# Optimization experiments

Measured on AMD Instinct MI355X. Metric: run time of the kernel, lower is better.

Reference implementation:

```python
import jax, jax.numpy as jnp
import numpy as np

N = 50000        # nodes
E = 800000       # edges (avg degree 16)
D_IN = 128
HID = 128
K = 3


def cheb_edge_weights(row, col, n):
    # PyG ChebConv sym normalization with assumed lambda_max = 2.0:
    # L_hat = (2/lambda_max) * (I - D^-1/2 A D^-1/2) - I = -D^-1/2 A D^-1/2 (zero diagonal)
    mask = (row != col).astype(jnp.float32)  # remove_self_loops
    deg = jax.ops.segment_sum(mask, row, num_segments=n)
    dinv = jnp.where(deg > 0.0, jax.lax.rsqrt(jnp.maximum(deg, 1.0)), 0.0)
    return -dinv[row] * dinv[col] * mask  # [E]


def cheb_conv(x, row, col, w_edge, W, b, n):
    # Chebyshev recursion: Tx0=x, Tx1=L_hat x, Tx_k = 2 L_hat Tx_{k-1} - Tx_{k-2}
    def prop(h):  # sparse L_hat @ h via gather + segment_sum
        return jax.ops.segment_sum(w_edge[:, None] * h[col], row, num_segments=n)

    Tx0 = x
    out = Tx0 @ W[0]
    Tx1 = prop(Tx0)
    out = out + Tx1 @ W[1]
    for k in range(2, W.shape[0]):
        Tx2 = 2.0 * prop(Tx1) - Tx0
        out = out + Tx2 @ W[k]
        Tx0, Tx1 = Tx1, Tx2
    return out + b


def setup_inputs() -> dict:
    key = jax.random.key(0)
    ks = jax.random.split(key, 8)
    x = jax.random.normal(ks[0], (N, D_IN), dtype=jnp.float32)
    ei = jax.random.randint(ks[1], (2, E), 0, N, dtype=jnp.int32)
    s = 0.05
    W1 = jax.random.normal(ks[2], (K, D_IN, HID), dtype=jnp.float32) * s
    b1 = jnp.zeros((HID,), dtype=jnp.float32)
    W2 = jax.random.normal(ks[3], (K, HID, HID), dtype=jnp.float32) * s
    b2 = jnp.zeros((HID,), dtype=jnp.float32)
    W3 = jax.random.normal(ks[4], (K, HID, HID), dtype=jnp.float32) * s
    b3 = jnp.zeros((HID,), dtype=jnp.float32)
    return {"x": x, "ei": ei, "W1": W1, "b1": b1, "W2": W2, "b2": b2, "W3": W3, "b3": b3}


def reference(x, ei, W1, b1, W2, b2, W3, b3):
    row, col = ei[0], ei[1]
    w_edge = cheb_edge_weights(row, col, N)
    # layer chain: ChebConv -> ReLU -> dropout (eval mode: identity)
    h = jax.nn.relu(cheb_conv(x, row, col, w_edge, W1, b1, N))
    h = jax.nn.relu(cheb_conv(h, row, col, w_edge, W2, b2, N))
    h = jax.nn.relu(cheb_conv(h, row, col, w_edge, W3, b3, N))
    return h
```

## Files before the change

kernel.cpp:

```cpp
#include <hip/hip_runtime.h>
#include <hip/hip_bf16.h>

#define DFEAT 128

typedef short bf16x8 __attribute__((ext_vector_type(8)));
typedef float f32x4  __attribute__((ext_vector_type(4)));
typedef unsigned short u16x8 __attribute__((ext_vector_type(8)));

__device__ __forceinline__ unsigned bf16r(float f) {
    unsigned u = __float_as_uint(f);
    u += 0x7fffu + ((u >> 16) & 1u);
    return u >> 16;
}
__device__ __forceinline__ unsigned pack_bf16(float lo, float hi) {
    return bf16r(lo) | (bf16r(hi) << 16);
}
__device__ __forceinline__ float blo(unsigned v) { return __uint_as_float(v << 16); }
__device__ __forceinline__ float bhi(unsigned v) { return __uint_as_float(v & 0xffff0000u); }
__device__ __forceinline__ float f16w(unsigned cw) {
    unsigned short wb = (unsigned short)(cw >> 16);
    _Float16 hf; __builtin_memcpy(&hf, &wb, 2);
    return (float)hf;
}

__global__ void deg_kernel(const int* __restrict__ ei, int* __restrict__ deg8, int E, int N) {
    int e = blockIdx.x * blockDim.x + threadIdx.x;
    if (e < E) {
        int r = ei[e];
        int c = ei[E + e];
        if (r != c) atomicAdd(&deg8[(blockIdx.x & 7) * N + r], 1);
    }
}

__global__ __launch_bounds__(1024) void scan1_kernel(const int* __restrict__ deg8,
                                                     int* __restrict__ poff,
                                                     int* __restrict__ row_ptr,
                                                     int* __restrict__ bsum,
                                                     float* __restrict__ dinv, int n) {
    __shared__ int wsums[16];
    int t = threadIdx.x;
    int idx = blockIdx.x * 1024 + t;
    int tot = 0;
    if (idx < n) {
        int run = 0;
        #pragma unroll
        for (int p = 0; p < 8; ++p) {
            int d = deg8[p * n + idx];
            poff[p * n + idx] = run;
            run += d;
        }
        tot = run;
        dinv[idx] = (tot > 0) ? rsqrtf((float)tot) : 0.f;
    }
    int vi = tot;
    #pragma unroll
    for (int off = 1; off < 64; off <<= 1) {
        int x = __shfl_up(vi, off);
        if ((t & 63) >= off) vi += x;
    }
    if ((t & 63) == 63) wsums[t >> 6] = vi;
    __syncthreads();
    if (t < 16) {
        int s = wsums[t];
        int si = s;
        #pragma unroll
        for (int off = 1; off < 16; off <<= 1) {
            int x = __shfl_up(si, off);
            if (t >= off) si += x;
        }
        wsums[t] = si - s;
        if (t == 15) bsum[blockIdx.x] = si;
    }
    __syncthreads();
    if (idx < n) row_ptr[idx + 1] = wsums[t >> 6] + vi;
}

__global__ void scan2_kernel(int* __restrict__ bsum, int nb) {
    int t = threadIdx.x;
    int carry = 0;
    for (int base = 0; base < nb; base += 64) {
        int v = (base + t < nb) ? bsum[base + t] : 0;
        int vi = v;
        #pragma unroll
        for (int off = 1; off < 64; off <<= 1) {
            int x = __shfl_up(vi, off);
            if (t >= off) vi += x;
        }
        if (base + t < nb) bsum[base + t] = carry + vi - v;
        carry += __shfl(vi, 63);
    }
}

__global__ __launch_bounds__(1024) void scan3_kernel(int* __restrict__ row_ptr,
                                                     const int* __restrict__ bsum, int n) {
    int idx = blockIdx.x * 1024 + threadIdx.x;
    if (idx == 0) row_ptr[0] = 0;
    if (idx < n) row_ptr[idx + 1] += bsum[blockIdx.x];
}

__global__ void fill_kernel(const int* __restrict__ ei, const int* __restrict__ row_ptr,
                            const int* __restrict__ poff, int* __restrict__ fillc8,
                            const float* __restrict__ dinv,
                            unsigned* __restrict__ e_cw, int E, int N) {
    int e = blockIdx.x * blockDim.x + threadIdx.x;
    if (e < E) {
        int r = ei[e];
        int c = ei[E + e];
        if (r != c) {
            int p = blockIdx.x & 7;
            int k = atomicAdd(&fillc8[p * N + r], 1);
            int pos = row_ptr[r] + poff[p * N + r] + k;
            float w = -dinv[r] * dinv[c];
            _Float16 hf = (_Float16)w;
            unsigned short wb;
            __builtin_memcpy(&wb, &hf, 2);
            e_cw[pos] = (unsigned)c | ((unsigned)wb << 16);
        }
    }
}

__global__ void conv_kernel(const float2* __restrict__ x, unsigned* __restrict__ xb, int npk,
                            const float* __restrict__ W1, const float* __restrict__ W2,
                            const float* __restrict__ W3, unsigned short* __restrict__ Wt) {
    int id = blockIdx.x * blockDim.x + threadIdx.x;
    if (id < npk) {
        float2 v = x[id];
        xb[id] = pack_bf16(v.x, v.y);
        return;
    }
    int id2 = id - npk;
    const int PER = 3 * DFEAT * DFEAT;
    if (id2 < 3 * PER) {
        int layer = id2 / PER;
        int rem = id2 - layer * PER;
        const float* W = (layer == 0) ? W1 : ((layer == 1) ? W2 : W3);
        int seg = rem >> 14;
        int k   = (rem >> 7) & 127;
        int nn  = rem & 127;
        Wt[layer * PER + (seg << 14) + (nn << 7) + k] = (unsigned short)bf16r(W[rem]);
    }
}

__global__ __launch_bounds__(256) void prop_bf16_kernel(
    const uint2* __restrict__ hin2, const uint2* __restrict__ sub2,
    uint2* __restrict__ hout2,
    const int* __restrict__ row_ptr, const unsigned* __restrict__ e_cw,
    float alpha, int n)
{
    int wv = __builtin_amdgcn_readfirstlane(threadIdx.x >> 6);
    int node = blockIdx.x * 4 + wv;
    if (node >= n) return;
    const int lane = threadIdx.x & 63;
    const int h = lane >> 5;
    const int s = lane & 31;
    int rs = row_ptr[node];
    int re = row_ptr[node + 1];

    float a0 = 0.f, a1 = 0.f, a2 = 0.f, a3 = 0.f;

    for (int j = rs; j < re; j += 24) {
        uint2 vv[12]; float wv2[12];
        #pragma unroll
        for (int u = 0; u < 12; ++u) {
            int i0 = j + 2 * u;
            unsigned cw0 = (i0     < re) ? e_cw[i0]     : 0u;
            unsigned cw1 = (i0 + 1 < re) ? e_cw[i0 + 1] : 0u;
            unsigned cw = h ? cw1 : cw0;
            wv2[u] = f16w(cw);
            vv[u] = hin2[(size_t)(cw & 0xffffu) * 32 + s];
        }
        #pragma unroll
        for (int u = 0; u < 12; ++u) {
            float w = wv2[u];
            a0 += w * blo(vv[u].x);  a1 += w * bhi(vv[u].x);
            a2 += w * blo(vv[u].y);  a3 += w * bhi(vv[u].y);
        }
    }
    a0 += __shfl_xor(a0, 32);
    a1 += __shfl_xor(a1, 32);
    a2 += __shfl_xor(a2, 32);
    a3 += __shfl_xor(a3, 32);

    a0 *= alpha; a1 *= alpha; a2 *= alpha; a3 *= alpha;
    size_t rowoff = (size_t)node * 32 + s;
    if (sub2) {
        uint2 sv = sub2[rowoff];
        a0 -= blo(sv.x);  a1 -= bhi(sv.x);
        a2 -= blo(sv.y);  a3 -= bhi(sv.y);
    }
    if (h == 0) {
        uint2 o;
        o.x = pack_bf16(a0, a1);
        o.y = pack_bf16(a2, a3);
        hout2[rowoff] = o;
    }
}

#define WPAD 136
__global__ __launch_bounds__(256) void gemm3_mfma_kernel(
    const unsigned short* __restrict__ X0, const unsigned short* __restrict__ X1,
    const unsigned short* __restrict__ X2,
    const unsigned short* __restrict__ Wt, const float* __restrict__ bias,
    void* __restrict__ out, int n, int out_bf16)
{
    __shared__ unsigned short Ws[DFEAT * WPAD];
    const int t    = threadIdx.x;
    const int wave = t >> 6;
    const int lane = t & 63;
    const int quad = lane >> 4;
    const int l16  = lane & 15;

    const int row_base = blockIdx.x * 128 + wave * 32;
    int r0 = row_base + l16;       if (r0 >= n) r0 = n - 1;
    int r1 = row_base + 16 + l16;  if (r1 >= n) r1 = n - 1;

    const unsigned short* Xps[3] = {X0, X1, X2};

    f32x4 acc[2][8];
    #pragma unroll
    for (int tt = 0; tt < 2; ++tt)
        #pragma unroll
        for (int c = 0; c < 8; ++c) acc[tt][c] = (f32x4){0.f, 0.f, 0.f, 0.f};

    const int srow = t >> 1;
    const int shalf = (t & 1) * 64;

    #pragma unroll
    for (int seg = 0; seg < 3; ++seg) {
        __syncthreads();
        const unsigned short* Wp = Wt + (seg << 14);
        #pragma unroll
        for (int i = 0; i < 8; ++i) {
            *(u16x8*)&Ws[srow * WPAD + shalf + i * 8] =
                *(const u16x8*)&Wp[srow * DFEAT + shalf + i * 8];
        }
        __syncthreads();
        const unsigned short* A0 = Xps[seg] + (size_t)r0 * DFEAT;
        const unsigned short* A1 = Xps[seg] + (size_t)r1 * DFEAT;
        #pragma unroll
        for (int kk = 0; kk < 4; ++kk) {
            const int ko = kk * 32 + quad * 8;
            bf16x8 a0 = *(const bf16x8*)(A0 + ko);
            bf16x8 a1 = *(const bf16x8*)(A1 + ko);
            #pragma unroll
            for (int c = 0; c < 8; ++c) {
                bf16x8 b = *(const bf16x8*)&Ws[(c * 16 + l16) * WPAD + ko];
                acc[0][c] = __builtin_amdgcn_mfma_f32_16x16x32_bf16(a0, b, acc[0][c], 0, 0, 0);
                acc[1][c] = __builtin_amdgcn_mfma_f32_16x16x32_bf16(a1, b, acc[1][c], 0, 0, 0);
            }
        }
    }

    #pragma unroll
    for (int tt = 0; tt < 2; ++tt) {
        int orow0 = blockIdx.x * 128 + wave * 32 + tt * 16 + quad * 4;
        #pragma unroll
        for (int c = 0; c < 8; ++c) {
            int col = c * 16 + l16;
            float bv = bias[col];
            #pragma unroll
            for (int r = 0; r < 4; ++r) {
                int orow = orow0 + r;
                if (orow < n) {
                    float v = fmaxf(acc[tt][c][r] + bv, 0.f);
                    if (out_bf16)
                        ((unsigned short*)out)[(size_t)orow * DFEAT + col] = (unsigned short)bf16r(v);
                    else
                        ((float*)out)[(size_t)orow * DFEAT + col] = v;
                }
            }
        }
    }
}

extern "C" void kernel_launch(void* const* d_in, const int* in_sizes, int n_in,
                              void* d_out, int out_size, void* d_ws, size_t ws_size,
                              hipStream_t stream) {
    const float* x  = (const float*)d_in[0];
    const int*   ei = (const int*)d_in[1];
    const float* W1 = (const float*)d_in[2];
    const float* b1 = (const float*)d_in[3];
    const float* W2 = (const float*)d_in[4];
    const float* b2 = (const float*)d_in[5];
    const float* W3 = (const float*)d_in[6];
    const float* b3 = (const float*)d_in[7];

    const int N = in_sizes[0] / DFEAT;
    const int E = in_sizes[1] / 2;
    const int NPK = N * (DFEAT / 2);
    const int NB = (N + 1023) / 1024;

    unsigned* xb  = (unsigned*)d_ws;
    unsigned* t1b = xb  + NPK;
    unsigned* t2b = t1b + NPK;
    unsigned* ab  = t2b + NPK;
    unsigned short* wt = (unsigned short*)(ab + NPK);
    int*   deg8    = (int*)(wt + 3 * 3 * DFEAT * DFEAT);
    int*   fillc8  = deg8 + 8 * N;
    int*   poff    = fillc8 + 8 * N;
    int*   row_ptr = poff + 8 * N;
    float* dinv    = (float*)(row_ptr + (N + 1));
    unsigned* e_cw = (unsigned*)(dinv + N);
    int*   bsum    = (int*)(e_cw + E);

    hipMemsetAsync(deg8, 0, sizeof(int) * 16 * N, stream);

    deg_kernel<<<(E + 255) / 256, 256, 0, stream>>>(ei, deg8, E, N);
    scan1_kernel<<<NB, 1024, 0, stream>>>(deg8, poff, row_ptr, bsum, dinv, N);
    scan2_kernel<<<1, 64, 0, stream>>>(bsum, NB);
    scan3_kernel<<<NB, 1024, 0, stream>>>(row_ptr, bsum, N);
    fill_kernel<<<(E + 255) / 256, 256, 0, stream>>>(ei, row_ptr, poff, fillc8, dinv, e_cw, E, N);

    const int WELEM = 3 * DFEAT * DFEAT;
    const int CONVT = NPK + 3 * WELEM;
    conv_kernel<<<(CONVT + 255) / 256, 256, 0, stream>>>(
        (const float2*)x, xb, NPK, W1, W2, W3, wt);

    const float* bl[3] = {b1, b2, b3};
    const unsigned* hin = xb;
    const int prop_grid = (N + 3) / 4;
    const int gemm_grid = (N + 127) / 128;
    for (int l = 0; l < 3; ++l) {
        prop_bf16_kernel<<<prop_grid, 256, 0, stream>>>(
            (const uint2*)hin, nullptr, (uint2*)t1b, row_ptr, e_cw, 1.f, N);
        prop_bf16_kernel<<<prop_grid, 256, 0, stream>>>(
            (const uint2*)t1b, (const uint2*)hin, (uint2*)t2b, row_ptr, e_cw, 2.f, N);
        void* hout = (l == 2) ? d_out : (void*)ab;
        gemm3_mfma_kernel<<<gemm_grid, 256, 0, stream>>>(
            (const unsigned short*)hin, (const unsigned short*)t1b, (const unsigned short*)t2b,
            wt + l * WELEM, bl[l], hout, N, (l == 2) ? 0 : 1);
        hin = ab;
    }
}
```

Before: 402.1 us.

## Fuse CSR build scans into single-pass decoupled scan, fold memset into conv kernel

Replaces the three-kernel scan (block scan, carry scan, add-back) with one kernel that chains block prefixes through a status array using flag-tagged atomics. The hipMemsetAsync is removed; zeroing of the degree counters and status words moves into the conversion kernel's grid-stride loop. The fill kernel now bumps the poff array directly as its cursor, so the separate fill-counter array is no longer needed. This cuts launches and memory traffic in graph preprocessing. The chained scan relies on blocks running in order, since each block spins on its predecessor's flag.

New measurement: 425.7 us. 1.06x slower.

```diff
diff --git a/kernel.cpp b/kernel.cpp
--- a/kernel.cpp
+++ b/kernel.cpp
@@ -23,106 +23,15 @@
     return (float)hf;
 }
 
-__global__ void deg_kernel(const int* __restrict__ ei, int* __restrict__ deg8, int E, int N) {
-    int e = blockIdx.x * blockDim.x + threadIdx.x;
-    if (e < E) {
-        int r = ei[e];
-        int c = ei[E + e];
-        if (r != c) atomicAdd(&deg8[(blockIdx.x & 7) * N + r], 1);
-    }
-}
-
-__global__ __launch_bounds__(1024) void scan1_kernel(const int* __restrict__ deg8,
-                                                     int* __restrict__ poff,
-                                                     int* __restrict__ row_ptr,
-                                                     int* __restrict__ bsum,
-                                                     float* __restrict__ dinv, int n) {
-    __shared__ int wsums[16];
-    int t = threadIdx.x;
-    int idx = blockIdx.x * 1024 + t;
-    int tot = 0;
-    if (idx < n) {
-        int run = 0;
-        #pragma unroll
-        for (int p = 0; p < 8; ++p) {
-            int d = deg8[p * n + idx];
-            poff[p * n + idx] = run;
-            run += d;
-        }
-        tot = run;
-        dinv[idx] = (tot > 0) ? rsqrtf((float)tot) : 0.f;
-    }
-    int vi = tot;
-    #pragma unroll
-    for (int off = 1; off < 64; off <<= 1) {
-        int x = __shfl_up(vi, off);
-        if ((t & 63) >= off) vi += x;
-    }
-    if ((t & 63) == 63) wsums[t >> 6] = vi;
-    __syncthreads();
-    if (t < 16) {
-        int s = wsums[t];
-        int si = s;
-        #pragma unroll
-        for (int off = 1; off < 16; off <<= 1) {
-            int x = __shfl_up(si, off);
-            if (t >= off) si += x;
-        }
-        wsums[t] = si - s;
-        if (t == 15) bsum[blockIdx.x] = si;
-    }
-    __syncthreads();
-    if (idx < n) row_ptr[idx + 1] = wsums[t >> 6] + vi;
-}
-
-__global__ void scan2_kernel(int* __restrict__ bsum, int nb) {
-    int t = threadIdx.x;
-    int carry = 0;
-    for (int base = 0; base < nb; base += 64) {
-        int v = (base + t < nb) ? bsum[base + t] : 0;
-        int vi = v;
-        #pragma unroll
-        for (int off = 1; off < 64; off <<= 1) {
-            int x = __shfl_up(vi, off);
-            if (t >= off) vi += x;
-        }
-        if (base + t < nb) bsum[base + t] = carry + vi - v;
-        carry += __shfl(vi, 63);
-    }
-}
-
-__global__ __launch_bounds__(1024) void scan3_kernel(int* __restrict__ row_ptr,
-                                                     const int* __restrict__ bsum, int n) {
-    int idx = blockIdx.x * 1024 + threadIdx.x;
-    if (idx == 0) row_ptr[0] = 0;
-    if (idx < n) row_ptr[idx + 1] += bsum[blockIdx.x];
-}
-
-__global__ void fill_kernel(const int* __restrict__ ei, const int* __restrict__ row_ptr,
-                            const int* __restrict__ poff, int* __restrict__ fillc8,
-                            const float* __restrict__ dinv,
-                            unsigned* __restrict__ e_cw, int E, int N) {
-    int e = blockIdx.x * blockDim.x + threadIdx.x;
-    if (e < E) {
-        int r = ei[e];
-        int c = ei[E + e];
-        if (r != c) {
-            int p = blockIdx.x & 7;
-            int k = atomicAdd(&fillc8[p * N + r], 1);
-            int pos = row_ptr[r] + poff[p * N + r] + k;
-            float w = -dinv[r] * dinv[c];
-            _Float16 hf = (_Float16)w;
-            unsigned short wb;
-            __builtin_memcpy(&wb, &hf, 2);
-            e_cw[pos] = (unsigned)c | ((unsigned)wb << 16);
-        }
-    }
-}
-
 __global__ void conv_kernel(const float2* __restrict__ x, unsigned* __restrict__ xb, int npk,
                             const float* __restrict__ W1, const float* __restrict__ W2,
-                            const float* __restrict__ W3, unsigned short* __restrict__ Wt) {
+                            const float* __restrict__ W3, unsigned short* __restrict__ Wt,
+                            int* __restrict__ deg8, unsigned long long* __restrict__ status,
+                            int N, int nb) {
     int id = blockIdx.x * blockDim.x + threadIdx.x;
+    int gstride = gridDim.x * blockDim.x;
+    for (int i = id; i < 8 * N; i += gstride) deg8[i] = 0;
+    if (id < nb) status[id] = 0ULL;
     if (id < npk) {
         float2 v = x[id];
         xb[id] = pack_bf16(v.x, v.y);
@@ -138,6 +47,93 @@
         int k   = (rem >> 7) & 127;
         int nn  = rem & 127;
         Wt[layer * PER + (seg << 14) + (nn << 7) + k] = (unsigned short)bf16r(W[rem]);
+    }
+}
+
+__global__ void deg_kernel(const int* __restrict__ ei, int* __restrict__ deg8, int E, int N) {
+    int e = blockIdx.x * blockDim.x + threadIdx.x;
+    if (e < E) {
+        int r = ei[e];
+        int c = ei[E + e];
+        if (r != c) atomicAdd(&deg8[(blockIdx.x & 7) * N + r], 1);
+    }
+}
+
+#define SFLAG 0x8000000000000000ULL
+__global__ __launch_bounds__(1024) void scan_kernel(
+    const int* __restrict__ deg8, int* __restrict__ poff, int* __restrict__ row_ptr,
+    unsigned long long* __restrict__ status, float* __restrict__ dinv, int n)
+{
+    __shared__ int wsums[16];
+    __shared__ int s_total;
+    __shared__ int s_prev;
+    const int b = blockIdx.x;
+    const int t = threadIdx.x;
+    int idx = b * 1024 + t;
+    int tot = 0;
+    if (idx < n) {
+        int run = 0;
+        #pragma unroll
+        for (int p = 0; p < 8; ++p) {
+            int d = deg8[p * n + idx];
+            poff[p * n + idx] = run;
+            run += d;
+        }
+        tot = run;
+        dinv[idx] = (tot > 0) ? rsqrtf((float)tot) : 0.f;
+    }
+    int vi = tot;
+    #pragma unroll
+    for (int off = 1; off < 64; off <<= 1) {
+        int xs = __shfl_up(vi, off);
+        if ((t & 63) >= off) vi += xs;
+    }
+    if ((t & 63) == 63) wsums[t >> 6] = vi;
+    __syncthreads();
+    if (t < 16) {
+        int s = wsums[t];
+        int si = s;
+        #pragma unroll
+        for (int off = 1; off < 16; off <<= 1) {
+            int xs = __shfl_up(si, off);
+            if (t >= off) si += xs;
+        }
+        wsums[t] = si - s;
+        if (t == 15) s_total = si;
+    }
+    __syncthreads();
+    if (t == 0) {
+        int prev = 0;
+        if (b > 0) {
+            unsigned long long v;
+            do { v = atomicAdd(&status[b - 1], 0ULL); } while (!(v & SFLAG));
+            prev = (int)(v & 0x7fffffffULL);
+        }
+        atomicExch(&status[b], SFLAG | (unsigned long long)(unsigned)(prev + s_total));
+        s_prev = prev;
+    }
+    __syncthreads();
+    if (idx < n) row_ptr[idx + 1] = s_prev + wsums[t >> 6] + vi;
+    if (b == 0 && t == 0) row_ptr[0] = 0;
+}
+
+__global__ void fill_kernel(const int* __restrict__ ei, const int* __restrict__ row_ptr,
+                            int* __restrict__ poff, const float* __restrict__ dinv,
+                            unsigned* __restrict__ e_cw, int E, int N) {
+    int e = blockIdx.x * blockDim.x + threadIdx.x;
+    if (e < E) {
+        int r = ei[e];
+        int c = ei[E + e];
+        if (r != c) {
+            int p = blockIdx.x & 7;
+            int k = atomicAdd(&poff[p * N + r], 1);
+            int pos = row_ptr[r] + k;
+            float w = -dinv[r] * dinv[c];
+            _Float16 hf = (_Float16)w;
+            unsigned short wb;
+            __builtin_memcpy(&wb, &hf, 2);
+            e_cw[pos] = (unsigned)c | ((unsigned)wb << 16);
+        }
     }
 }
 
@@ -296,25 +292,19 @@
     unsigned* ab  = t2b + NPK;
     unsigned short* wt = (unsigned short*)(ab + NPK);
     int*   deg8    = (int*)(wt + 3 * 3 * DFEAT * DFEAT);
-    int*   fillc8  = deg8 + 8 * N;
-    int*   poff    = fillc8 + 8 * N;
+    int*   poff    = deg8 + 8 * N;
     int*   row_ptr = poff + 8 * N;
-    float* dinv    = (float*)(row_ptr + (N + 1));
+    float* dinv    = (float*)(row_ptr + (N + 2));
     unsigned* e_cw = (unsigned*)(dinv + N);
-    int*   bsum    = (int*)(e_cw + E);
-
-    hipMemsetAsync(deg8, 0, sizeof(int) * 16 * N, stream);
-
-    deg_kernel<<<(E + 255) / 256, 256, 0, stream>>>(ei, deg8, E, N);
-    scan1_kernel<<<NB, 1024, 0, stream>>>(deg8, poff, row_ptr, bsum, dinv, N);
-    scan2_kernel<<<1, 64, 0, stream>>>(bsum, NB);
-    scan3_kernel<<<NB, 1024, 0, stream>>>(row_ptr, bsum, N);
-    fill_kernel<<<(E + 255) / 256, 256, 0, stream>>>(ei, row_ptr, poff, fillc8, dinv, e_cw, E, N);
+    unsigned long long* status = (unsigned long long*)((char*)(e_cw + E) + 16);
 
     const int WELEM = 3 * DFEAT * DFEAT;
     const int CONVT = NPK + 3 * WELEM;
     conv_kernel<<<(CONVT + 255) / 256, 256, 0, stream>>>(
-        (const float2*)x, xb, NPK, W1, W2, W3, wt);
+        (const float2*)x, xb, NPK, W1, W2, W3, wt, deg8, status, N, NB);
+    deg_kernel<<<(E + 255) / 256, 256, 0, stream>>>(ei, deg8, E, N);
+    scan_kernel<<<NB, 1024, 0, stream>>>(deg8, poff, row_ptr, status, dinv, N);
+    fill_kernel<<<(E + 255) / 256, 256, 0, stream>>>(ei, row_ptr, poff, dinv, e_cw, E, N);
 
     const float* bl[3] = {b1, b2, b3};
     const unsigned* hin = xb;
```

## Fold Chebyshev recurrence into weights and drop memset and fill counters

Applied to the files above, without the earlier changes.

Rewrites out = T0 W0 + T1 W1 + (2 L T1 - T0) W2 as T0 (W0 - W2) + T1 W1 + (L T1)(2 W2). The second propagation no longer reads and subtracts the previous features, which saves one feature-matrix read per layer. The memset is replaced by zeroing deg8 inside the conversion kernel, and the fill kernel reuses poff as its atomic counter, removing the separate fillc8 array. Precision shifts slightly because the combined weights are rounded to bf16 and the un-scaled L·T1 is stored in bf16. Correctness depends on poff holding exclusive offsets after the scan.

Result: faster. 389.9 us (-3.0%).

```diff
diff --git a/kernel.cpp b/kernel.cpp
--- a/kernel.cpp
+++ b/kernel.cpp
@@ -21,6 +21,35 @@
     unsigned short wb = (unsigned short)(cw >> 16);
     _Float16 hf; __builtin_memcpy(&hf, &wb, 2);
     return (float)hf;
+}
+
+
+__global__ void conv_kernel(const float2* __restrict__ x, unsigned* __restrict__ xb, int npk,
+                            const float* __restrict__ W1, const float* __restrict__ W2,
+                            const float* __restrict__ W3, unsigned short* __restrict__ Wt,
+                            int* __restrict__ deg8, int N) {
+    int id = blockIdx.x * blockDim.x + threadIdx.x;
+    int gstride = gridDim.x * blockDim.x;
+    for (int i = id; i < 8 * N; i += gstride) deg8[i] = 0;
+    if (id < npk) {
+        float2 v = x[id];
+        xb[id] = pack_bf16(v.x, v.y);
+        return;
+    }
+    int id2 = id - npk;
+    const int PER = 3 * DFEAT * DFEAT;
+    if (id2 < 3 * PER) {
+        int layer = id2 / PER;
+        int rem = id2 - layer * PER;
+        const float* W = (layer == 0) ? W1 : ((layer == 1) ? W2 : W3);
+        int seg = rem >> 14;
+        int k   = (rem >> 7) & 127;
+        int nn  = rem & 127;
+        float w = W[rem];
+        if (seg == 0) w -= W[rem + 2 * DFEAT * DFEAT];
+        else if (seg == 2) w *= 2.f;
+        Wt[layer * PER + (seg << 14) + (nn << 7) + k] = (unsigned short)bf16r(w);
+    }
 }
 
 __global__ void deg_kernel(const int* __restrict__ ei, int* __restrict__ deg8, int E, int N) {
@@ -99,8 +128,7 @@
 }
 
 __global__ void fill_kernel(const int* __restrict__ ei, const int* __restrict__ row_ptr,
-                            const int* __restrict__ poff, int* __restrict__ fillc8,
-                            const float* __restrict__ dinv,
+                            int* __restrict__ poff, const float* __restrict__ dinv,
                             unsigned* __restrict__ e_cw, int E, int N) {
     int e = blockIdx.x * blockDim.x + threadIdx.x;
     if (e < E) {
@@ -108,8 +136,8 @@
         int c = ei[E + e];
         if (r != c) {
             int p = blockIdx.x & 7;
-            int k = atomicAdd(&fillc8[p * N + r], 1);
-            int pos = row_ptr[r] + poff[p * N + r] + k;
+            int k = atomicAdd(&poff[p * N + r], 1);
+            int pos = row_ptr[r] + k;
             float w = -dinv[r] * dinv[c];
             _Float16 hf = (_Float16)w;
             unsigned short wb;
@@ -119,33 +147,9 @@
     }
 }
 
-__global__ void conv_kernel(const float2* __restrict__ x, unsigned* __restrict__ xb, int npk,
-                            const float* __restrict__ W1, const float* __restrict__ W2,
-                            const float* __restrict__ W3, unsigned short* __restrict__ Wt) {
-    int id = blockIdx.x * blockDim.x + threadIdx.x;
-    if (id < npk) {
-        float2 v = x[id];
-        xb[id] = pack_bf16(v.x, v.y);
-        return;
-    }
-    int id2 = id - npk;
-    const int PER = 3 * DFEAT * DFEAT;
-    if (id2 < 3 * PER) {
-        int layer = id2 / PER;
-        int rem = id2 - layer * PER;
-        const float* W = (layer == 0) ? W1 : ((layer == 1) ? W2 : W3);
-        int seg = rem >> 14;
-        int k   = (rem >> 7) & 127;
-        int nn  = rem & 127;
-        Wt[layer * PER + (seg << 14) + (nn << 7) + k] = (unsigned short)bf16r(W[rem]);
-    }
-}
-
 __global__ __launch_bounds__(256) void prop_bf16_kernel(
-    const uint2* __restrict__ hin2, const uint2* __restrict__ sub2,
-    uint2* __restrict__ hout2,
-    const int* __restrict__ row_ptr, const unsigned* __restrict__ e_cw,
-    float alpha, int n)
+    const uint2* __restrict__ hin2, uint2* __restrict__ hout2,
+    const int* __restrict__ row_ptr, const unsigned* __restrict__ e_cw, int n)
 {
     int wv = __builtin_amdgcn_readfirstlane(threadIdx.x >> 6);
     int node = blockIdx.x * 4 + wv;
@@ -181,18 +185,11 @@
     a2 += __shfl_xor(a2, 32);
     a3 += __shfl_xor(a3, 32);
 
-    a0 *= alpha; a1 *= alpha; a2 *= alpha; a3 *= alpha;
-    size_t rowoff = (size_t)node * 32 + s;
-    if (sub2) {
-        uint2 sv = sub2[rowoff];
-        a0 -= blo(sv.x);  a1 -= bhi(sv.x);
-        a2 -= blo(sv.y);  a3 -= bhi(sv.y);
-    }
     if (h == 0) {
         uint2 o;
         o.x = pack_bf16(a0, a1);
         o.y = pack_bf16(a2, a3);
-        hout2[rowoff] = o;
+        hout2[(size_t)node * 32 + s] = o;
     }
 }
 
@@ -296,25 +293,21 @@
     unsigned* ab  = t2b + NPK;
     unsigned short* wt = (unsigned short*)(ab + NPK);
     int*   deg8    = (int*)(wt + 3 * 3 * DFEAT * DFEAT);
-    int*   fillc8  = deg8 + 8 * N;
-    int*   poff    = fillc8 + 8 * N;
+    int*   poff    = deg8 + 8 * N;
     int*   row_ptr = poff + 8 * N;
-    float* dinv    = (float*)(row_ptr + (N + 1));
+    float* dinv    = (float*)(row_ptr + (N + 2));
     unsigned* e_cw = (unsigned*)(dinv + N);
     int*   bsum    = (int*)(e_cw + E);
 
-    hipMemsetAsync(deg8, 0, sizeof(int) * 16 * N, stream);
-
+    const int WELEM = 3 * DFEAT * DFEAT;
+    const int CONVT = NPK + 3 * WELEM;
+    conv_kernel<<<(CONVT + 255) / 256, 256, 0, stream>>>(
+        (const float2*)x, xb, NPK, W1, W2, W3, wt, deg8, N);
     deg_kernel<<<(E + 255) / 256, 256, 0, stream>>>(ei, deg8, E, N);
     scan1_kernel<<<NB, 1024, 0, stream>>>(deg8, poff, row_ptr, bsum, dinv, N);
     scan2_kernel<<<1, 64, 0, stream>>>(bsum, NB);
     scan3_kernel<<<NB, 1024, 0, stream>>>(row_ptr, bsum, N);
-    fill_kernel<<<(E + 255) / 256, 256, 0, stream>>>(ei, row_ptr, poff, fillc8, dinv, e_cw, E, N);
-
-    const int WELEM = 3 * DFEAT * DFEAT;
-    const int CONVT = NPK + 3 * WELEM;
-    conv_kernel<<<(CONVT + 255) / 256, 256, 0, stream>>>(
-        (const float2*)x, xb, NPK, W1, W2, W3, wt);
+    fill_kernel<<<(E + 255) / 256, 256, 0, stream>>>(ei, row_ptr, poff, dinv, e_cw, E, N);
 
     const float* bl[3] = {b1, b2, b3};
     const unsigned* hin = xb;
@@ -322,9 +315,9 @@
     const int gemm_grid = (N + 127) / 128;
     for (int l = 0; l < 3; ++l) {
         prop_bf16_kernel<<<prop_grid, 256, 0, stream>>>(
-            (const uint2*)hin, nullptr, (uint2*)t1b, row_ptr, e_cw, 1.f, N);
+            (const uint2*)hin, (uint2*)t1b, row_ptr, e_cw, N);
         prop_bf16_kernel<<<prop_grid, 256, 0, stream>>>(
-            (const uint2*)t1b, (const uint2*)hin, (uint2*)t2b, row_ptr, e_cw, 2.f, N);
+            (const uint2*)t1b, (uint2*)t2b, row_ptr, e_cw, N);
         void* hout = (l == 2) ? d_out : (void*)ab;
         gemm3_mfma_kernel<<<gemm_grid, 256, 0, stream>>>(
             (const unsigned short*)hin, (const unsigned short*)t1b, (const unsigned short*)t2b,
```
